# Optimization experiments

Measured on AMD Instinct MI355X. Metric: run time of the kernel, lower is better.

The kernel has to match this reference:

```python
import jax, jax.numpy as jnp
import numpy as np

B, C, E, H = 8, 2048, 256, 64
N_AGENTS = 4
KAPPA = 0.9
MASKED = True


def _decay_xi_delta(dones):
    """Vectorized equivalent of get_decay_matrix / get_xi / delta.

    dones: [B, C] bool. Timestep dones are dones[:, ::N_AGENTS] -> [B, T].
    The original Python loop builds mask[b,n,m] = exists i with ts_done[b,i]
    and n >= i and m < i, i.e. a done strictly after m and at-or-before n.
    That equals (inclusive_cumsum[n] - inclusive_cumsum[m]) > 0.
    """
    ts = dones[:, ::N_AGENTS]                      # [B, T]
    T = ts.shape[1]
    csum = jnp.cumsum(ts.astype(jnp.int32), axis=1)            # inclusive
    blocked = (csum[:, :, None] - csum[:, None, :]) > 0        # [B, T, T]
    ts_mask = (~blocked).astype(jnp.float32)

    n = jnp.arange(T)
    diff = n[:, None] - n[None, :]
    dm = jnp.where(diff >= 0, KAPPA ** diff.astype(jnp.float32), 0.0)  # [T, T]
    dm = dm[None, :, :] * ts_mask                               # [B, T, T]
    # repeat_interleave over both time axes -> per-agent [B, C, C]
    dm = jnp.repeat(jnp.repeat(dm, N_AGENTS, axis=1), N_AGENTS, axis=2)
    if MASKED:
        Cfull = dm.shape[-1]
        dm = dm * jnp.tril(jnp.ones((Cfull, Cfull), dm.dtype))[None]

    # xi: kappa^(t+1) before the first done, 0 after (per timestep, repeated per agent)
    has_done = jnp.any(ts, axis=1, keepdims=True)               # [B, 1]
    first = jnp.argmax(ts.astype(jnp.float32), axis=1, keepdims=True)
    first = jnp.where(has_done, first, T)                       # [B, 1]
    t_idx = jnp.arange(T)[None, :]                              # [1, T]
    xi = (KAPPA ** (t_idx + 1).astype(jnp.float32)) * (t_idx < first).astype(jnp.float32)
    xi = jnp.repeat(xi, N_AGENTS, axis=1)[:, :, None]           # [B, C, 1]

    delta = (~jnp.any(ts, axis=1)).astype(jnp.float32)[:, None, None]  # [B,1,1]
    return dm, xi, delta


def setup_inputs() -> dict:
    key = jax.random.key(0)
    ks = jax.random.split(key, 8)
    return {
        "key_in": jax.random.normal(ks[0], (B, C, E), jnp.float32),
        "query": jax.random.normal(ks[1], (B, C, E), jnp.float32),
        "value": jax.random.normal(ks[2], (B, C, E), jnp.float32),
        "hstate": jax.random.normal(ks[3], (B, H, H), jnp.float32),
        "dones": jax.random.randint(ks[4], (B, C), 0, 2).astype(bool),
        "w_q": jax.random.normal(ks[5], (E, H), jnp.float32) / np.sqrt(E).astype(np.float32),
        "w_k": jax.random.normal(ks[6], (E, H), jnp.float32) / np.sqrt(E).astype(np.float32),
        "w_v": jax.random.normal(ks[7], (E, H), jnp.float32) / np.sqrt(E).astype(np.float32),
    }


def reference(key_in, query, value, hstate, dones, w_q, w_k, w_v):
    q = query @ w_q                                  # [B, C, H]
    k = key_in @ w_k                                 # [B, C, H]
    v = value @ w_v                                  # [B, C, H]

    dm, xi, delta = _decay_xi_delta(dones)           # [B,C,C], [B,C,1], [B,1,1]
    T = C // N_AGENTS
    chunk_decay = KAPPA ** T

    # next_hstate = k^T @ (v * last_row_of_decay^T) + hstate * chunk_decay * delta
    next_h = jnp.einsum('bch,bcd->bhd', k, v * dm[:, -1, :, None]) \
        + hstate * chunk_decay * delta

    cross = jnp.einsum('bch,bhd->bcd', q, hstate) * xi         # [B, C, H]
    scores = jnp.einsum('bch,bmh->bcm', q, k) * dm              # [B, C, C]
    inner = jnp.einsum('bcm,bmd->bcd', scores, v)               # [B, C, H]
    return inner + cross, next_h
```

## Files before the change

### kernel.cpp

```cpp
#include <hip/hip_runtime.h>
#include <hip/hip_bf16.h>
#include <cstddef>

#define B_ 8
#define C_ 2048
#define E_ 256
#define H_ 64
#define T_ 512
#define NA 4
#define KAPPA 0.9f
#define LOG2_KAPPA (-0.15200309344504997f)
#define KAPPA_T 3.73302e-24f

typedef __attribute__((ext_vector_type(8))) short bf16x8;
typedef __attribute__((ext_vector_type(4))) float f32x4;

__device__ inline unsigned short f2bfu(float x) {
    unsigned u = __builtin_bit_cast(unsigned, x);
    u += 0x7fff + ((u >> 16) & 1);
    return (unsigned short)(u >> 16);
}
__device__ inline short f2bf(float x) { return (short)f2bfu(x); }
__device__ inline float bf2f(unsigned short u) {
    return __builtin_bit_cast(float, (unsigned)u << 16);
}
__device__ inline unsigned pack2bf(float lo, float hi) {
    return (unsigned)f2bfu(lo) | ((unsigned)f2bfu(hi) << 16);
}

__global__ __launch_bounds__(256) void prep_kernel(
    const float* __restrict__ w_q, const float* __restrict__ w_k,
    const float* __restrict__ w_v, short* __restrict__ wt,
    const unsigned char* __restrict__ raw, int* __restrict__ s_tab)
{
    const int t = threadIdx.x;
    if (blockIdx.x < 12) {
        const int mat = blockIdx.x >> 2;
        const int k0  = (blockIdx.x & 3) * 64;
        const float* W = (mat == 0) ? w_q : (mat == 1) ? w_k : w_v;
        __shared__ float tile[64][67];
#pragma unroll
        for (int pass = 0; pass < 16; ++pass) {
            int idx = pass * 256 + t;
            int r = idx >> 6, c = idx & 63;
            tile[r][c] = W[(size_t)(k0 + r) * H_ + c];
        }
        __syncthreads();
#pragma unroll
        for (int pass = 0; pass < 16; ++pass) {
            int idx = pass * 256 + t;
            int d = idx >> 6, c = idx & 63;
            wt[(size_t)mat * (H_ * E_) + (size_t)d * E_ + k0 + c] = f2bf(tile[c][d]);
        }
    } else {
        const int b    = blockIdx.x - 12;
        const int lane = t & 63;
        const int w    = t >> 6;
        __shared__ int f;
        __shared__ unsigned long long msk[8];
        if (t == 0) f = 0;
        __syncthreads();
        {
            const uint4* dp = (const uint4*)raw;
            unsigned acc = 0;
#pragma unroll
            for (int i = 0; i < 4; ++i) {
                uint4 v = dp[t + 256 * i];
                acc |= (v.x | v.y | v.z | v.w) & 0xFFFFFF00u;
            }
            if (acc) f = 1;
        }
        __syncthreads();
        const int stride = f ? 1 : 4;
        const unsigned char* drow = raw + (size_t)b * C_ * stride;
#pragma unroll
        for (int cc = 0; cc < 2; ++cc) {
            const int c = 2 * w + cc;
            const int n = c * 64 + lane;
            unsigned long long m = __ballot(drow[(size_t)(4 * n) * stride] != 0);
            if (lane == 0) msk[c] = m;
        }
        __syncthreads();
#pragma unroll
        for (int cc = 0; cc < 2; ++cc) {
            const int c = 2 * w + cc;
            const int n = c * 64 + lane;
            unsigned long long lowmask =
                (lane == 63) ? ~0ULL : ((1ULL << (lane + 1)) - 1ULL);
            unsigned long long m_le = msk[c] & lowmask;
            int s = -1;
            if (m_le) {
                s = c * 64 + (63 - __builtin_clzll(m_le));
            } else {
                for (int c2 = c - 1; c2 >= 0; --c2)
                    if (msk[c2]) { s = c2 * 64 + (63 - __builtin_clzll(msk[c2])); break; }
            }
            s_tab[b * T_ + n] = s;
        }
    }
}

__global__ __launch_bounds__(256) void proj_mfma(
    const float* __restrict__ key_in, const float* __restrict__ query,
    const float* __restrict__ value, const short* __restrict__ wt,
    unsigned short* __restrict__ qp, unsigned short* __restrict__ kp,
    unsigned short* __restrict__ vp)
{
    const int mat = blockIdx.y;
    const float* A; unsigned short* O16;
    if (mat == 0)      { A = query;  O16 = qp; }
    else if (mat == 1) { A = key_in; O16 = kp; }
    else               { A = value;  O16 = vp; }

    __shared__ short Wt[64][264];

    const int t    = threadIdx.x;
    const int b    = blockIdx.x & 7;
    const int rb   = blockIdx.x >> 3;
    const int row0 = b * C_ + rb * 64;
    const int lane = t & 63;
    const int mt   = t >> 6;
    const int lr   = lane & 15;
    const int lg   = lane >> 4;

    const short* wsrc = wt + (size_t)mat * (H_ * E_);
#pragma unroll
    for (int pass = 0; pass < 8; ++pass) {
        int idx = pass * 2048 + t * 8;
        int d = idx >> 8, k = idx & 255;
        *(bf16x8*)&Wt[d][k] = *(const bf16x8*)&wsrc[idx];
    }
    __syncthreads();

    const float* arow = &A[(size_t)(row0 + mt * 16 + lr) * E_ + lg * 8];

    f32x4 acc[4] = {};
#pragma unroll
    for (int kc = 0; kc < 8; ++kc) {
        f32x4 x0 = *(const f32x4*)(arow + kc * 32);
        f32x4 x1 = *(const f32x4*)(arow + kc * 32 + 4);
        bf16x8 af;
        af[0] = f2bf(x0[0]); af[1] = f2bf(x0[1]);
        af[2] = f2bf(x0[2]); af[3] = f2bf(x0[3]);
        af[4] = f2bf(x1[0]); af[5] = f2bf(x1[1]);
        af[6] = f2bf(x1[2]); af[7] = f2bf(x1[3]);
#pragma unroll
        for (int nt = 0; nt < 4; ++nt) {
            bf16x8 bfrag = *(const bf16x8*)&Wt[nt * 16 + lr][kc * 32 + lg * 8];
            acc[nt] = __builtin_amdgcn_mfma_f32_16x16x32_bf16(af, bfrag, acc[nt], 0, 0, 0);
        }
    }

    const int odd   = lr & 1;
    const int rbase = row0 + mt * 16 + lg * 4;
#pragma unroll
    for (int nt = 0; nt < 4; ++nt) {
        const int cp = nt * 16 + (lr & ~1);
        float x0 = acc[nt][0], x1 = acc[nt][1], x2 = acc[nt][2], x3 = acc[nt][3];
        float y0 = __shfl_xor(x0, 1), y1 = __shfl_xor(x1, 1);
        float y2 = __shfl_xor(x2, 1), y3 = __shfl_xor(x3, 1);
        if (!odd) {
            *(unsigned*)&O16[(size_t)(rbase + 0) * H_ + cp] = pack2bf(x0, y0);
            *(unsigned*)&O16[(size_t)(rbase + 1) * H_ + cp] = pack2bf(x1, y1);
        } else {
            *(unsigned*)&O16[(size_t)(rbase + 2) * H_ + cp] = pack2bf(y2, x2);
            *(unsigned*)&O16[(size_t)(rbase + 3) * H_ + cp] = pack2bf(y3, x3);
        }
    }
}

__global__ __launch_bounds__(256) void out_kernel(
    const unsigned short* __restrict__ qp, const unsigned short* __restrict__ kp,
    const unsigned short* __restrict__ vp, const float* __restrict__ hs,
    const int* __restrict__ s_tab,
    float* __restrict__ out0, float* __restrict__ outh)
{
    const int t    = threadIdx.x;
    const int lane = t & 63;
    const int w    = t >> 6;
    const int bid  = blockIdx.x;

    if (bid < 1024) {
        const int b = bid & 7;
        const int n = (bid >> 3) * 4 + w;
        const int a = lane >> 4;
        const int g = lane & 15;

        const int st = s_tab[b * T_ + n];
        const int s  = (st < 0) ? 0 : st;

        const unsigned short* kb = kp + (size_t)b * C_ * H_;
        const unsigned short* vb = vp + (size_t)b * C_ * H_;
        ushort4 qu = *(const ushort4*)&qp[((size_t)b * C_ + 4 * n + a) * H_ + 4 * g];
        f32x4 q4 = { bf2f(qu.x), bf2f(qu.y), bf2f(qu.z), bf2f(qu.w) };

        f32x4 acc = {};
#pragma unroll
        for (int ma = 0; ma < NA; ++ma) {
            const int m = 4 * n + ma;
            ushort4 ku = *(const ushort4*)&kb[(size_t)m * H_ + 4 * g];
            float p = q4[0] * bf2f(ku.x) + q4[1] * bf2f(ku.y)
                    + q4[2] * bf2f(ku.z) + q4[3] * bf2f(ku.w);
            p += __shfl_xor(p, 1); p += __shfl_xor(p, 2);
            p += __shfl_xor(p, 4); p += __shfl_xor(p, 8);
            if (ma <= a) {
                ushort4 vu = *(const ushort4*)&vb[(size_t)m * H_ + 4 * g];
                acc[0] += p * bf2f(vu.x); acc[1] += p * bf2f(vu.y);
                acc[2] += p * bf2f(vu.z); acc[3] += p * bf2f(vu.w);
            }
        }
        float decay = KAPPA;
        for (int mt = n - 1; mt >= s; --mt) {
#pragma unroll
            for (int ma = 0; ma < NA; ++ma) {
                const int m = 4 * mt + ma;
                ushort4 ku = *(const ushort4*)&kb[(size_t)m * H_ + 4 * g];
                float p = q4[0] * bf2f(ku.x) + q4[1] * bf2f(ku.y)
                        + q4[2] * bf2f(ku.z) + q4[3] * bf2f(ku.w);
                p += __shfl_xor(p, 1); p += __shfl_xor(p, 2);
                p += __shfl_xor(p, 4); p += __shfl_xor(p, 8);
                p *= decay;
                ushort4 vu = *(const ushort4*)&vb[(size_t)m * H_ + 4 * g];
                acc[0] += p * bf2f(vu.x); acc[1] += p * bf2f(vu.y);
                acc[2] += p * bf2f(vu.z); acc[3] += p * bf2f(vu.w);
            }
            decay *= KAPPA;
        }
        if (st < 0) {
            const float xi = exp2f(LOG2_KAPPA * (float)(n + 1));
            const float* hsb = hs + (size_t)b * H_ * H_;
            f32x4 cacc = {};
#pragma unroll
            for (int h = 0; h < H_; ++h) {
                float qh = __shfl(q4[h & 3], (a << 4) + (h >> 2));
                f32x4 h4 = *(const f32x4*)&hsb[h * H_ + 4 * g];
                cacc[0] += qh * h4[0]; cacc[1] += qh * h4[1];
                cacc[2] += qh * h4[2]; cacc[3] += qh * h4[3];
            }
            acc[0] += xi * cacc[0]; acc[1] += xi * cacc[1];
            acc[2] += xi * cacc[2]; acc[3] += xi * cacc[3];
        }
        *(f32x4*)&out0[((size_t)b * C_ + 4 * n + a) * H_ + 4 * g] = acc;
    } else {
        const int j = bid - 1024;
        const int b = j & 7;
        const int h = (j >> 3) * 4 + w;
        const int d = lane;

        const int st = s_tab[b * T_ + (T_ - 1)];
        const int s  = (st < 0) ? 0 : st;

        const unsigned short* kb = kp + (size_t)b * C_ * H_;
        const unsigned short* vb = vp + (size_t)b * C_ * H_;
        float acc = 0.f, wdec = 1.f;
        for (int mt = T_ - 1; mt >= s; --mt) {
#pragma unroll
            for (int ma = 0; ma < NA; ++ma) {
                const int m = 4 * mt + ma;
                acc += wdec * bf2f(kb[(size_t)m * H_ + h]) *
                              bf2f(vb[(size_t)m * H_ + d]);
            }
            wdec *= KAPPA;
        }
        if (st < 0)
            acc += hs[((size_t)b * H_ + h) * H_ + d] * KAPPA_T;
        outh[((size_t)b * H_ + h) * H_ + d] = acc;
    }
}

extern "C" void kernel_launch(void* const* d_in, const int* in_sizes, int n_in,
                              void* d_out, int out_size, void* d_ws, size_t ws_size,
                              hipStream_t stream)
{
    const float* key_in = (const float*)d_in[0];
    const float* query  = (const float*)d_in[1];
    const float* value  = (const float*)d_in[2];
    const float* hstate = (const float*)d_in[3];
    const unsigned char* dones = (const unsigned char*)d_in[4];
    const float* w_q = (const float*)d_in[5];
    const float* w_k = (const float*)d_in[6];
    const float* w_v = (const float*)d_in[7];

    unsigned short* qp = (unsigned short*)d_ws;
    unsigned short* kp = qp + (size_t)B_ * C_ * H_;
    unsigned short* vp = kp + (size_t)B_ * C_ * H_;
    short*          wt = (short*)(vp + (size_t)B_ * C_ * H_);
    int*         s_tab = (int*)(wt + 3 * H_ * E_);

    prep_kernel<<<20, 256, 0, stream>>>(w_q, w_k, w_v, wt, dones, s_tab);
    dim3 pgrid(B_ * C_ / 64, 3);
    proj_mfma<<<pgrid, 256, 0, stream>>>(key_in, query, value, wt, qp, kp, vp);
    out_kernel<<<1024 + 128, 256, 0, stream>>>(
        qp, kp, vp, hstate, s_tab,
        (float*)d_out, (float*)d_out + (size_t)B_ * C_ * H_);
}
```

Measured before the change: 29.81 us.

## Load projection weights via direct global-to-LDS copies with XOR swizzle and prefetch A

The prep kernel now writes the transposed bf16 weights in an XOR-swizzled byte layout, so the projection kernel can copy them straight into unpadded shared memory with global_load_lds instead of staging through registers. The swizzle is meant to avoid LDS bank conflicts that padding previously handled. The projection loop also software-prefetches the next A chunk before the barrier and during each MFMA step, which overlaps global load latency with compute. The cost is higher register pressure and a layout coupling between the two kernels.

```diff
diff --git a/kernel.cpp b/kernel.cpp
--- a/kernel.cpp
+++ b/kernel.cpp
@@ -28,9 +28,14 @@
     return (unsigned)f2bfu(lo) | ((unsigned)f2bfu(hi) << 16);
 }
 
+#define GLOAD_LDS16(gp, lp)                                                    \
+    __builtin_amdgcn_global_load_lds(                                          \
+        (const __attribute__((address_space(1))) void*)(gp),                   \
+        (__attribute__((address_space(3))) void*)(lp), 16, 0, 0)
+
 __global__ __launch_bounds__(256) void prep_kernel(
     const float* __restrict__ w_q, const float* __restrict__ w_k,
-    const float* __restrict__ w_v, short* __restrict__ wt,
+    const float* __restrict__ w_v, char* __restrict__ wt,
     const unsigned char* __restrict__ raw, int* __restrict__ s_tab)
 {
     const int t = threadIdx.x;
@@ -38,6 +43,7 @@
         const int mat = blockIdx.x >> 2;
         const int k0  = (blockIdx.x & 3) * 64;
         const float* W = (mat == 0) ? w_q : (mat == 1) ? w_k : w_v;
+        char* wm = wt + (size_t)mat * 32768;
         __shared__ float tile[64][67];
 #pragma unroll
         for (int pass = 0; pass < 16; ++pass) {
@@ -50,7 +56,8 @@
         for (int pass = 0; pass < 16; ++pass) {
             int idx = pass * 256 + t;
             int d = idx >> 6, c = idx & 63;
-            wt[(size_t)mat * (H_ * E_) + (size_t)d * E_ + k0 + c] = f2bf(tile[c][d]);
+            int byte = (d << 9) + ((((k0 + c) << 1)) ^ ((d & 7) << 4));
+            *(short*)(wm + byte) = f2bf(tile[c][d]);
         }
     } else {
         const int b    = blockIdx.x - 12;
@@ -102,7 +109,7 @@
 
 __global__ __launch_bounds__(256) void proj_mfma(
     const float* __restrict__ key_in, const float* __restrict__ query,
-    const float* __restrict__ value, const short* __restrict__ wt,
+    const float* __restrict__ value, const char* __restrict__ wt,
     unsigned short* __restrict__ qp, unsigned short* __restrict__ kp,
     unsigned short* __restrict__ vp)
 {
@@ -112,7 +119,7 @@
     else if (mat == 1) { A = key_in; O16 = kp; }
     else               { A = value;  O16 = vp; }
 
-    __shared__ short Wt[64][264];
+    __shared__ __align__(16) char Wt[64 * 512];
 
     const int t    = threadIdx.x;
     const int b    = blockIdx.x & 7;
@@ -122,23 +129,27 @@
     const int mt   = t >> 6;
     const int lr   = lane & 15;
     const int lg   = lane >> 4;
-
-    const short* wsrc = wt + (size_t)mat * (H_ * E_);
-#pragma unroll
-    for (int pass = 0; pass < 8; ++pass) {
-        int idx = pass * 2048 + t * 8;
-        int d = idx >> 8, k = idx & 255;
-        *(bf16x8*)&Wt[d][k] = *(const bf16x8*)&wsrc[idx];
-    }
+    const int swz  = (lr & 7) << 4;
+
+    const char* wsrc = wt + (size_t)mat * 32768;
+#pragma unroll
+    for (int pass = 0; pass < 8; ++pass)
+        GLOAD_LDS16(wsrc + pass * 4096 + t * 16, Wt + pass * 4096 + t * 16);
+
+    const float* arow = &A[(size_t)(row0 + mt * 16 + lr) * E_ + lg * 8];
+
+    f32x4 x0 = *(const f32x4*)(arow);
+    f32x4 x1 = *(const f32x4*)(arow + 4);
     __syncthreads();
 
-    const float* arow = &A[(size_t)(row0 + mt * 16 + lr) * E_ + lg * 8];
-
     f32x4 acc[4] = {};
 #pragma unroll
     for (int kc = 0; kc < 8; ++kc) {
-        f32x4 x0 = *(const f32x4*)(arow + kc * 32);
-        f32x4 x1 = *(const f32x4*)(arow + kc * 32 + 4);
+        f32x4 n0, n1;
+        if (kc < 7) {
+            n0 = *(const f32x4*)(arow + (kc + 1) * 32);
+            n1 = *(const f32x4*)(arow + (kc + 1) * 32 + 4);
+        }
         bf16x8 af;
         af[0] = f2bf(x0[0]); af[1] = f2bf(x0[1]);
         af[2] = f2bf(x0[2]); af[3] = f2bf(x0[3]);
@@ -146,9 +157,11 @@
         af[6] = f2bf(x1[2]); af[7] = f2bf(x1[3]);
 #pragma unroll
         for (int nt = 0; nt < 4; ++nt) {
-            bf16x8 bfrag = *(const bf16x8*)&Wt[nt * 16 + lr][kc * 32 + lg * 8];
+            bf16x8 bfrag = *(const bf16x8*)&Wt[((nt * 16 + lr) << 9) +
+                                               ((kc * 64 + lg * 16) ^ swz)];
             acc[nt] = __builtin_amdgcn_mfma_f32_16x16x32_bf16(af, bfrag, acc[nt], 0, 0, 0);
         }
+        x0 = n0; x1 = n1;
     }
 
     const int odd   = lr & 1;
@@ -156,15 +169,15 @@
 #pragma unroll
     for (int nt = 0; nt < 4; ++nt) {
         const int cp = nt * 16 + (lr & ~1);
-        float x0 = acc[nt][0], x1 = acc[nt][1], x2 = acc[nt][2], x3 = acc[nt][3];
-        float y0 = __shfl_xor(x0, 1), y1 = __shfl_xor(x1, 1);
-        float y2 = __shfl_xor(x2, 1), y3 = __shfl_xor(x3, 1);
+        float x0_ = acc[nt][0], x1_ = acc[nt][1], x2_ = acc[nt][2], x3_ = acc[nt][3];
+        float y0 = __shfl_xor(x0_, 1), y1 = __shfl_xor(x1_, 1);
+        float y2 = __shfl_xor(x2_, 1), y3 = __shfl_xor(x3_, 1);
         if (!odd) {
-            *(unsigned*)&O16[(size_t)(rbase + 0) * H_ + cp] = pack2bf(x0, y0);
-            *(unsigned*)&O16[(size_t)(rbase + 1) * H_ + cp] = pack2bf(x1, y1);
+            *(unsigned*)&O16[(size_t)(rbase + 0) * H_ + cp] = pack2bf(x0_, y0);
+            *(unsigned*)&O16[(size_t)(rbase + 1) * H_ + cp] = pack2bf(x1_, y1);
         } else {
-            *(unsigned*)&O16[(size_t)(rbase + 2) * H_ + cp] = pack2bf(y2, x2);
-            *(unsigned*)&O16[(size_t)(rbase + 3) * H_ + cp] = pack2bf(y3, x3);
+            *(unsigned*)&O16[(size_t)(rbase + 2) * H_ + cp] = pack2bf(y2, x2_);
+            *(unsigned*)&O16[(size_t)(rbase + 3) * H_ + cp] = pack2bf(y3, x3_);
         }
     }
 }
@@ -284,8 +297,8 @@
     unsigned short* qp = (unsigned short*)d_ws;
     unsigned short* kp = qp + (size_t)B_ * C_ * H_;
     unsigned short* vp = kp + (size_t)B_ * C_ * H_;
-    short*          wt = (short*)(vp + (size_t)B_ * C_ * H_);
-    int*         s_tab = (int*)(wt + 3 * H_ * E_);
+    char*           wt = (char*)(vp + (size_t)B_ * C_ * H_);
+    int*         s_tab = (int*)(wt + 3 * 32768);
 
     prep_kernel<<<20, 256, 0, stream>>>(w_q, w_k, w_v, wt, dones, s_tab);
     dim3 pgrid(B_ * C_ / 64, 3);
```

New measurement: 29.63 us, median of 4. About the same (-0.6%).
